# Optimization experiments

Hardware: AMD Instinct MI355X
Metric: run time of the kernel (lower is better)

The kernel has to match this reference:

```python
import jax, jax.numpy as jnp
import numpy as np
from jax import lax

B, L, D = 1024, 50, 128          # batch, max_seq_len, embed_dim
NV, NH = 8, 16                    # n_v vertical filters, n_h horizontal filters
NU, NI = 100000, 100000           # num_users, num_items


def setup_inputs() -> dict:
    key = jax.random.key(0)
    ks = jax.random.split(key, 9)
    return {
        "user_ids": jax.random.randint(ks[0], (B,), 0, NU),
        "item_seq": jax.random.randint(ks[1], (B, L), 0, NI),
        "user_emb": jax.random.normal(ks[2], (NU, D), jnp.float32) * 0.02,
        "item_emb": jax.random.normal(ks[3], (NI, D), jnp.float32) * 0.02,
        "vfilter": jax.random.normal(ks[4], (L, NV), jnp.float32) * 0.1,
        # hconv_w[i] holds the Conv2d(1, NH, (i+1, D)) weight, zero-padded to height L;
        # only rows [:i+1] are used for filter of height h=i+1.
        "hconv_w": jax.random.normal(ks[5], (L, NH, L, D), jnp.float32) * 0.05,
        "hconv_b": jax.random.normal(ks[6], (L, NH), jnp.float32) * 0.01,
        "fc_w": jax.random.normal(ks[7], (NV * D + NH * L, D), jnp.float32) * 0.02,
        "fc_b": jax.random.normal(ks[8], (D,), jnp.float32) * 0.01,
    }


def reference(user_ids, item_seq, user_emb, item_emb, vfilter, hconv_w, hconv_b, fc_w, fc_b):
    P_u = user_emb[user_ids]                 # [B, D]
    E = item_emb[item_seq]                   # [B, L, D]

    # vertical conv: (E^T @ V)^T flattened as (v major, d minor) -> [B, NV*D]
    o_v = jnp.einsum('bld,lv->bvd', E, vfilter).reshape(E.shape[0], -1)

    # horizontal convs: one per kernel height h = 1..L (structurally distinct kernels)
    x = E[:, None, :, :]                     # NCHW: [B, 1, L, D]
    o_h = []
    for i in range(L):
        h = i + 1
        w = hconv_w[i, :, :h, :][:, None, :, :]   # OIHW: [NH, 1, h, D]
        c = lax.conv_general_dilated(
            x, w, window_strides=(1, 1), padding='VALID',
            dimension_numbers=('NCHW', 'OIHW', 'NCHW'))[..., 0]   # [B, NH, L-h+1]
        c = jax.nn.relu(c + hconv_b[i][None, :, None])
        o_h.append(jnp.max(c, axis=2))            # max-pool over all valid positions
    o_h = jnp.concatenate(o_h, axis=1)            # [B, NH*L]

    o = jnp.concatenate([o_v, o_h], axis=1)       # [B, NV*D + NH*L]
    z = jax.nn.relu(o @ fc_w + fc_b)              # [B, D]
    return jnp.concatenate([z, P_u], axis=1)      # [B, 2*D]
```

## Files before the change

kernel.cpp:

```cpp
#include <hip/hip_runtime.h>
#include <hip/hip_bf16.h>
#include <stdint.h>

#define B_   1024
#define L_   50
#define D_   128
#define NV_  8
#define NH_  16
#define KFC  1824

typedef __bf16 bf16x8 __attribute__((ext_vector_type(8)));
typedef float  f32x4  __attribute__((ext_vector_type(4)));

static __device__ __forceinline__ bf16x8 as_bf16x8(uint4 u) {
  return __builtin_bit_cast(bf16x8, u);
}

static __device__ __forceinline__ unsigned short f2b(float x) {
  unsigned u = __float_as_uint(x);
  return (unsigned short)((u + 0x7FFFu + ((u >> 16) & 1u)) >> 16);
}

#define OV_BYTES  ((size_t)B_ * KFC * 4)
#define E3OFF     (OV_BYTES)
#define E3_KS     3342336
#define E3_BG     52224
#define E3SZ      ((size_t)4 * E3_KS)
#define W2OFF     (E3OFF + E3SZ)
#define W2SZ      ((size_t)1275 * 4096)
#define NEED_FULL (W2OFF + W2SZ)

__global__ void ck_kP(const int* __restrict__ uids, const float* __restrict__ uemb,
                      float* __restrict__ out) {
  int b = blockIdx.x, d = threadIdx.x;
  out[(size_t)b * 256 + 128 + d] = uemb[(size_t)uids[b] * D_ + d];
}

__global__ void ck_kZ(float* __restrict__ out) {
  int i = blockIdx.x * 256 + threadIdx.x;
  int b = i >> 7, d = i & 127;
  out[(size_t)b * 256 + d] = 0.f;
}

__global__ void ck_kAB(const int* __restrict__ item_seq, const float* __restrict__ item_emb,
                       const float* __restrict__ vf, char* __restrict__ ws) {
  int b = blockIdx.x, tid = threadIdx.x;
  __shared__ float E[L_][D_];
  __shared__ float VF[L_][NV_];
  __shared__ int sidx[L_];
  if (tid < L_) sidx[tid] = item_seq[b * L_ + tid];
  for (int c = tid; c < L_ * NV_; c += 256) VF[c / NV_][c % NV_] = vf[c];
  __syncthreads();
  for (int c = tid; c < 1600; c += 256) {
    int l = c >> 5, ch = c & 31;
    *(float4*)&E[l][ch * 4] = *(const float4*)(item_emb + (size_t)sidx[l] * D_ + ch * 4);
  }
  __syncthreads();
  char* eg = ws + E3OFF + (size_t)(b >> 4) * E3_BG + (b & 15) * 64;
  #pragma unroll
  for (int it = 0; it < 4; ++it) {
    int c = it * 256 + tid;
    if (c < 816) {
      int ks = c / 204, rem = c - ks * 204;
      uint4 v = make_uint4(0, 0, 0, 0);
      int row, gq;
      if (rem < 200) {
        row = rem >> 2; gq = rem & 3;
        float4 f0 = *(const float4*)&E[row][ks * 32 + gq * 8];
        float4 f1 = *(const float4*)&E[row][ks * 32 + gq * 8 + 4];
        v.x = f2b(f0.x) | ((unsigned)f2b(f0.y) << 16);
        v.y = f2b(f0.z) | ((unsigned)f2b(f0.w) << 16);
        v.z = f2b(f1.x) | ((unsigned)f2b(f1.y) << 16);
        v.w = f2b(f1.z) | ((unsigned)f2b(f1.w) << 16);
      } else {
        row = 50; gq = rem - 200;
      }
      *(uint4*)(eg + (size_t)ks * E3_KS + row * 1024 + gq * 16) = v;
    }
  }
  int d = tid & 127, half = tid >> 7;
  float acc[4] = {0.f, 0.f, 0.f, 0.f};
  for (int l = 0; l < L_; ++l) {
    float e = E[l][d];
    #pragma unroll
    for (int vv = 0; vv < 4; ++vv) acc[vv] += e * VF[l][half * 4 + vv];
  }
  float* o = (float*)ws + (size_t)b * KFC;
  #pragma unroll
  for (int vv = 0; vv < 4; ++vv) o[(half * 4 + vv) * D_ + d] = acc[vv];
}

__global__ void ck_kW2(const float* __restrict__ hw, char* __restrict__ ws) {
  int p = blockIdx.x, tid = threadIdx.x;
  int ks = tid >> 6, l = tid & 63;
  int n = l & 15, gq = l >> 4;
  int i = (int)((sqrtf(8.0f * (float)p + 1.0f) - 1.0f) * 0.5f);
  while ((i + 1) * (i + 2) / 2 <= p) ++i;
  while (i * (i + 1) / 2 > p) --i;
  int j = p - i * (i + 1) / 2;
  const float* src = hw + ((size_t)(i * 16 + n) * 50 + j) * 128 + ks * 32 + gq * 8;
  float4 f0 = *(const float4*)(src);
  float4 f1 = *(const float4*)(src + 4);
  uint4 v;
  v.x = f2b(f0.x) | ((unsigned)f2b(f0.y) << 16);
  v.y = f2b(f0.z) | ((unsigned)f2b(f0.w) << 16);
  v.z = f2b(f1.x) | ((unsigned)f2b(f1.y) << 16);
  v.w = f2b(f1.z) | ((unsigned)f2b(f1.w) << 16);
  *(uint4*)(ws + W2OFF + (size_t)p * 4096 + tid * 16) = v;
}

#define MFMA_BF16 __builtin_amdgcn_mfma_f32_16x16x32_bf16

template<int NT4>
__device__ __forceinline__ void proc_item_g(const char* __restrict__ ebase,
    const char* __restrict__ bp0, int i, int t0, f32x4 (&acc)[8]) {
  bf16x8 win[8];
  #pragma unroll
  for (int q = 0; q < 8; ++q) {
    int s = t0 + q; s = s > 50 ? 50 : s;
    win[q] = as_bf16x8(*(const uint4*)(ebase + s * 1024));
  }
  uint4 breg[8];
  #pragma unroll
  for (int u = 0; u < 8; ++u)
    breg[u] = *(const uint4*)(bp0 + (size_t)(u <= i ? u : 0) * 4096);

  for (int j0 = 0; j0 <= i; j0 += 8) {
    #pragma unroll
    for (int u = 0; u < 8; ++u) {
      int j = j0 + u;
      if (j <= i) {
        bf16x8 bfr = as_bf16x8(breg[u]);
        acc[0] = MFMA_BF16(win[u], bfr, acc[0], 0, 0, 0);
        acc[1] = MFMA_BF16(win[(u + 1) & 7], bfr, acc[1], 0, 0, 0);
        acc[2] = MFMA_BF16(win[(u + 2) & 7], bfr, acc[2], 0, 0, 0);
        acc[3] = MFMA_BF16(win[(u + 3) & 7], bfr, acc[3], 0, 0, 0);
        int sn = t0 + j + 8; sn = sn > 50 ? 50 : sn;
        win[u] = as_bf16x8(*(const uint4*)(ebase + sn * 1024));
        if (NT4 == 8) {
          acc[4] = MFMA_BF16(win[(u + 4) & 7], bfr, acc[4], 0, 0, 0);
          acc[5] = MFMA_BF16(win[(u + 5) & 7], bfr, acc[5], 0, 0, 0);
          acc[6] = MFMA_BF16(win[(u + 6) & 7], bfr, acc[6], 0, 0, 0);
          acc[7] = MFMA_BF16(win[(u + 7) & 7], bfr, acc[7], 0, 0, 0);
        }
        if (j + 8 <= i) breg[u] = *(const uint4*)(bp0 + (size_t)(j + 8) * 4096);
      }
    }
  }
}

__launch_bounds__(256, 4)
__global__ void ck_kC6(const float* __restrict__ hconv_b, char* __restrict__ ws) {
  int tid = threadIdx.x;
  int wv = tid >> 6, lane = tid & 63;
  int r = lane & 15, gq = lane >> 4;
  int bid = (int)blockIdx.x;
  int g = bid & 63;
  int q = bid >> 6;
  int widx = q * 4 + wv;

  int rem = widx, i = -1, nt = 0, t0 = 0;
  for (int ii = 49; ii >= 0; --ii) {
    int nw = (57 - ii) >> 3;
    if (rem < nw) {
      i = ii;
      int ntb = 50 - ii - 8 * (nw - 1);
      nt = rem ? 8 : ntb;
      t0 = rem ? ntb + 8 * (rem - 1) : 0;
      break;
    }
    rem -= nw;
  }
  if (i < 0) return;
  int nt4 = (nt + 3) & ~3;

  const char* EG = ws + E3OFF + (size_t)g * E3_BG + r * 64 + gq * 16;
  const char* W2 = ws + W2OFF + (size_t)(i * (i + 1) / 2) * 4096 + lane * 16;
  float* o = (float*)ws;

  f32x4 acc[8];
  #pragma unroll
  for (int t = 0; t < 8; ++t) {
    acc[t][0] = 0.f; acc[t][1] = 0.f; acc[t][2] = 0.f; acc[t][3] = 0.f;
  }

  #pragma unroll
  for (int ks = 0; ks < 4; ++ks) {
    const char* ebase = EG + (size_t)ks * E3_KS;
    const char* bp0   = W2 + ks * 1024;
    if (nt4 == 4) proc_item_g<4>(ebase, bp0, i, t0, acc);
    else          proc_item_g<8>(ebase, bp0, i, t0, acc);
  }

  int b0 = g * 16;
  float bias = hconv_b[i * 16 + r];
  #pragma unroll
  for (int e = 0; e < 4; ++e) {
    float m = 0.f;
    #pragma unroll
    for (int tt = 0; tt < 8; ++tt)
      if (tt < nt) m = fmaxf(m, fmaxf(acc[tt][e] + bias, 0.f));
    atomicMax((unsigned*)&o[(size_t)(b0 + gq * 4 + e) * KFC + 1024 + i * 16 + r],
              __float_as_uint(m));
  }
}

__launch_bounds__(256)
__global__ void ck_kD(const float* __restrict__ fc_w, const float* __restrict__ fc_b,
                      const char* __restrict__ ws, float* __restrict__ out) {
  __shared__ char ldsD[10240];
  int b0 = blockIdx.x * 64, n0 = blockIdx.y * 16;
  int tid = threadIdx.x, w = tid >> 6, lane = tid & 63, r = lane & 15, gq = lane >> 4;
  const float* o = (const float*)ws;

  f32x4 acc; acc[0] = 0.f; acc[1] = 0.f; acc[2] = 0.f; acc[3] = 0.f;

  int rl = tid >> 2, ch = tid & 3;
  const float* asrc = o + (size_t)(b0 + rl) * KFC + ch * 8;
  int kk = tid >> 3, nn = tid & 7;

  float4 fa[4]; float fb[4];
  fa[0] = *(const float4*)(asrc);
  fa[1] = *(const float4*)(asrc + 4);
  fa[2] = *(const float4*)(asrc + 32);
  fa[3] = *(const float4*)(asrc + 36);
  fb[0] = fc_w[(size_t)kk * D_ + n0 + nn];
  fb[1] = fc_w[(size_t)kk * D_ + n0 + nn + 8];
  fb[2] = fc_w[(size_t)(32 + kk) * D_ + n0 + nn];
  fb[3] = fc_w[(size_t)(32 + kk) * D_ + n0 + nn + 8];

  int arow_off = rl * 64 + ((ch ^ (rl & 3)) << 4);
  int rloc = w * 16 + r;
  int ard = rloc * 64 + ((gq ^ (rloc & 3)) << 4);
  int brd = 8192 + r * 64 + ((gq ^ (r & 3)) << 4);
  int bw0 = 8192 + nn * 64 + (((kk >> 3) ^ (nn & 3)) << 4) + (kk & 7) * 2;
  int bw1 = 8192 + (nn + 8) * 64 + (((kk >> 3) ^ ((nn + 8) & 3)) << 4) + (kk & 7) * 2;

  for (int s = 0; s < 29; ++s) {
    int k1ok = (2 * s + 1) < 57;
    __syncthreads();
    #pragma unroll
    for (int sl = 0; sl < 2; ++sl) {
      uint4 v;
      v.x = f2b(fa[2*sl].x) | ((unsigned)f2b(fa[2*sl].y) << 16);
      v.y = f2b(fa[2*sl].z) | ((unsigned)f2b(fa[2*sl].w) << 16);
      v.z = f2b(fa[2*sl+1].x) | ((unsigned)f2b(fa[2*sl+1].y) << 16);
      v.w = f2b(fa[2*sl+1].z) | ((unsigned)f2b(fa[2*sl+1].w) << 16);
      *(uint4*)(ldsD + sl * 4096 + arow_off) = v;
      *(unsigned short*)(ldsD + sl * 1024 + bw0) = f2b(fb[2*sl]);
      *(unsigned short*)(ldsD + sl * 1024 + bw1) = f2b(fb[2*sl+1]);
    }
    __syncthreads();
    int kn0 = (2 * s + 2) * 32, kn1 = (2 * s + 3) * 32;
    if (kn0 < 1824) {
      fa[0] = *(const float4*)(asrc + kn0);
      fa[1] = *(const float4*)(asrc + kn0 + 4);
      fb[0] = fc_w[(size_t)(kn0 + kk) * D_ + n0 + nn];
      fb[1] = fc_w[(size_t)(kn0 + kk) * D_ + n0 + nn + 8];
    }
    if (kn1 < 1824) {
      fa[2] = *(const float4*)(asrc + kn1);
      fa[3] = *(const float4*)(asrc + kn1 + 4);
      fb[2] = fc_w[(size_t)(kn1 + kk) * D_ + n0 + nn];
      fb[3] = fc_w[(size_t)(kn1 + kk) * D_ + n0 + nn + 8];
    }
    bf16x8 a0  = as_bf16x8(*(const uint4*)(ldsD + ard));
    bf16x8 b0f = as_bf16x8(*(const uint4*)(ldsD + brd));
    acc = __builtin_amdgcn_mfma_f32_16x16x32_bf16(a0, b0f, acc, 0, 0, 0);
    if (k1ok) {
      bf16x8 a1  = as_bf16x8(*(const uint4*)(ldsD + 4096 + ard));
      bf16x8 b1f = as_bf16x8(*(const uint4*)(ldsD + 1024 + brd));
      acc = __builtin_amdgcn_mfma_f32_16x16x32_bf16(a1, b1f, acc, 0, 0, 0);
    }
  }

  float bias = fc_b[n0 + r];
  #pragma unroll
  for (int e = 0; e < 4; ++e) {
    int row = b0 + w * 16 + gq * 4 + e;
    out[(size_t)row * 256 + n0 + r] = fmaxf(acc[e] + bias, 0.f);
  }
}

extern "C" void kernel_launch(void* const* d_in, const int* in_sizes, int n_in,
                              void* d_out, int out_size, void* d_ws, size_t ws_size,
                              hipStream_t stream) {
  const int*   user_ids = (const int*)d_in[0];
  const int*   item_seq = (const int*)d_in[1];
  const float* user_emb = (const float*)d_in[2];
  const float* item_emb = (const float*)d_in[3];
  const float* vfilter  = (const float*)d_in[4];
  const float* hconv_w  = (const float*)d_in[5];
  const float* hconv_b  = (const float*)d_in[6];
  const float* fc_w     = (const float*)d_in[7];
  const float* fc_b     = (const float*)d_in[8];
  float* out = (float*)d_out;
  char*  ws  = (char*)d_ws;

  ck_kP<<<dim3(B_), dim3(128), 0, stream>>>(user_ids, user_emb, out);

  if (ws_size < NEED_FULL) {
    ck_kZ<<<dim3(512), dim3(256), 0, stream>>>(out);
    return;
  }

  hipMemsetAsync(ws, 0, OV_BYTES, stream);

  ck_kAB<<<dim3(B_), dim3(256), 0, stream>>>(item_seq, item_emb, vfilter, ws);
  ck_kW2<<<dim3(1275), dim3(256), 0, stream>>>(hconv_w, ws);
  ck_kC6<<<dim3(2944), dim3(256), 0, stream>>>(hconv_b, ws);
  ck_kD<<<dim3(16, 8), dim3(256), 0, stream>>>(fc_w, fc_b, ws, out);
}
```

Before: 174.9 us.

## Stage per-group embedding slices in LDS and distribute conv work via atomic counter

The horizontal-conv kernel now copies each 16-batch group's bf16 embedding slice into shared memory with global_load_lds and reads its sliding windows from LDS instead of global memory. It launches a persistent grid of 12 blocks per group with 8 waves each. Those blocks pull work items dynamically through a per-group atomic counter that is zeroed in the workspace. The intent is to cut repeated global/L2 reads of the same embedding data and to balance the uneven triangular workload. In exchange, every K-slice now needs extra block-wide barriers, and some waves idle when the remaining work is smaller than a block.

```diff
diff --git a/kernel.cpp b/kernel.cpp
--- a/kernel.cpp
+++ b/kernel.cpp
@@ -23,12 +23,17 @@
 
 #define OV_BYTES  ((size_t)B_ * KFC * 4)
 #define E3OFF     (OV_BYTES)
-#define E3_KS     3342336
 #define E3_BG     52224
+#define E3_KS     ((size_t)64 * E3_BG)
 #define E3SZ      ((size_t)4 * E3_KS)
 #define W2OFF     (E3OFF + E3SZ)
 #define W2SZ      ((size_t)1275 * 4096)
-#define NEED_FULL (W2OFF + W2SZ)
+#define CTR_OFF   (W2OFF + W2SZ)
+#define NEED_FULL (CTR_OFF + 256)
+
+#define GLD16(gsrc, ldst) __builtin_amdgcn_global_load_lds(                    \
+    (const __attribute__((address_space(1))) void*)(gsrc),                     \
+    (__attribute__((address_space(3))) void*)(ldst), 16, 0, 0)
 
 __global__ void ck_kP(const int* __restrict__ uids, const float* __restrict__ uemb,
                       float* __restrict__ out) {
@@ -111,14 +116,13 @@
 
 #define MFMA_BF16 __builtin_amdgcn_mfma_f32_16x16x32_bf16
 
-template<int NT4>
-__device__ __forceinline__ void proc_item_g(const char* __restrict__ ebase,
-    const char* __restrict__ bp0, int i, int t0, f32x4 (&acc)[8]) {
+__device__ __forceinline__ void proc8(const char* buf, const char* bp0,
+    int i, int t0, f32x4 (&acc)[8], int aoff) {
   bf16x8 win[8];
   #pragma unroll
   for (int q = 0; q < 8; ++q) {
     int s = t0 + q; s = s > 50 ? 50 : s;
-    win[q] = as_bf16x8(*(const uint4*)(ebase + s * 1024));
+    win[q] = as_bf16x8(*(const uint4*)(buf + s * 1024 + aoff));
   }
   uint4 breg[8];
   #pragma unroll
@@ -136,72 +140,92 @@
         acc[2] = MFMA_BF16(win[(u + 2) & 7], bfr, acc[2], 0, 0, 0);
         acc[3] = MFMA_BF16(win[(u + 3) & 7], bfr, acc[3], 0, 0, 0);
         int sn = t0 + j + 8; sn = sn > 50 ? 50 : sn;
-        win[u] = as_bf16x8(*(const uint4*)(ebase + sn * 1024));
-        if (NT4 == 8) {
-          acc[4] = MFMA_BF16(win[(u + 4) & 7], bfr, acc[4], 0, 0, 0);
-          acc[5] = MFMA_BF16(win[(u + 5) & 7], bfr, acc[5], 0, 0, 0);
-          acc[6] = MFMA_BF16(win[(u + 6) & 7], bfr, acc[6], 0, 0, 0);
-          acc[7] = MFMA_BF16(win[(u + 7) & 7], bfr, acc[7], 0, 0, 0);
-        }
+        win[u] = as_bf16x8(*(const uint4*)(buf + sn * 1024 + aoff));
+        acc[4] = MFMA_BF16(win[(u + 4) & 7], bfr, acc[4], 0, 0, 0);
+        acc[5] = MFMA_BF16(win[(u + 5) & 7], bfr, acc[5], 0, 0, 0);
+        acc[6] = MFMA_BF16(win[(u + 6) & 7], bfr, acc[6], 0, 0, 0);
+        acc[7] = MFMA_BF16(win[(u + 7) & 7], bfr, acc[7], 0, 0, 0);
         if (j + 8 <= i) breg[u] = *(const uint4*)(bp0 + (size_t)(j + 8) * 4096);
       }
     }
   }
 }
 
-__launch_bounds__(256, 4)
-__global__ void ck_kC6(const float* __restrict__ hconv_b, char* __restrict__ ws) {
+__launch_bounds__(512, 4)
+__global__ void ck_kC8(const float* __restrict__ hconv_b, char* __restrict__ ws) {
+  __shared__ __align__(16) char lds[E3_BG + 16];
+  int* bcast = (int*)(lds + E3_BG);
   int tid = threadIdx.x;
   int wv = tid >> 6, lane = tid & 63;
   int r = lane & 15, gq = lane >> 4;
-  int bid = (int)blockIdx.x;
-  int g = bid & 63;
-  int q = bid >> 6;
-  int widx = q * 4 + wv;
-
-  int rem = widx, i = -1, nt = 0, t0 = 0;
-  for (int ii = 49; ii >= 0; --ii) {
-    int nw = (57 - ii) >> 3;
-    if (rem < nw) {
-      i = ii;
-      int ntb = 50 - ii - 8 * (nw - 1);
-      nt = rem ? 8 : ntb;
-      t0 = rem ? ntb + 8 * (rem - 1) : 0;
-      break;
-    }
-    rem -= nw;
-  }
-  if (i < 0) return;
-  int nt4 = (nt + 3) & ~3;
-
-  const char* EG = ws + E3OFF + (size_t)g * E3_BG + r * 64 + gq * 16;
-  const char* W2 = ws + W2OFF + (size_t)(i * (i + 1) / 2) * 4096 + lane * 16;
+  int g = (int)blockIdx.x;
+  int aoff = r * 64 + gq * 16;
+
+  const char* EG = ws + E3OFF + (size_t)g * E3_BG;
+  const char* W2 = ws + W2OFF;
+  unsigned* ctr = (unsigned*)(ws + CTR_OFF) + g;
   float* o = (float*)ws;
 
-  f32x4 acc[8];
-  #pragma unroll
-  for (int t = 0; t < 8; ++t) {
-    acc[t][0] = 0.f; acc[t][1] = 0.f; acc[t][2] = 0.f; acc[t][3] = 0.f;
-  }
-
-  #pragma unroll
-  for (int ks = 0; ks < 4; ++ks) {
-    const char* ebase = EG + (size_t)ks * E3_KS;
-    const char* bp0   = W2 + ks * 1024;
-    if (nt4 == 4) proc_item_g<4>(ebase, bp0, i, t0, acc);
-    else          proc_item_g<8>(ebase, bp0, i, t0, acc);
-  }
-
-  int b0 = g * 16;
-  float bias = hconv_b[i * 16 + r];
-  #pragma unroll
-  for (int e = 0; e < 4; ++e) {
-    float m = 0.f;
-    #pragma unroll
-    for (int tt = 0; tt < 8; ++tt)
-      if (tt < nt) m = fmaxf(m, fmaxf(acc[tt][e] + bias, 0.f));
-    atomicMax((unsigned*)&o[(size_t)(b0 + gq * 4 + e) * KFC + 1024 + i * 16 + r],
-              __float_as_uint(m));
+  for (;;) {
+    if (tid == 0) bcast[0] = (int)atomicAdd(ctr, 8u);
+    #pragma unroll
+    for (int it = 0; it < 6; ++it)
+      GLD16(EG + (size_t)(it * 512 + tid) * 16, lds + (it * 512 + wv * 64) * 16);
+    if (wv < 3)
+      GLD16(EG + (size_t)(3072 + tid) * 16, lds + (3072 + wv * 64) * 16);
+    __syncthreads();
+    int base = bcast[0];
+    if (base >= 182) break;
+
+    int widx = base + wv;
+    int i = -1, nt = 0, t0 = 0;
+    int rem = widx;
+    for (int ii = 49; ii >= 0; --ii) {
+      int nw = (57 - ii) >> 3;
+      if (rem < nw) {
+        i = ii;
+        int ntb = 50 - ii - 8 * (nw - 1);
+        nt = rem ? 8 : ntb;
+        t0 = rem ? ntb + 8 * (rem - 1) : 0;
+        break;
+      }
+      rem -= nw;
+    }
+
+    f32x4 acc[8];
+    #pragma unroll
+    for (int t = 0; t < 8; ++t) {
+      acc[t][0] = 0.f; acc[t][1] = 0.f; acc[t][2] = 0.f; acc[t][3] = 0.f;
+    }
+    const char* bpb = W2 + (size_t)(i >= 0 ? i * (i + 1) / 2 : 0) * 4096 + lane * 16;
+
+    for (int ks = 0; ks < 4; ++ks) {
+      if (i >= 0) proc8(lds, bpb + ks * 1024, i, t0, acc, aoff);
+      __syncthreads();
+      if (ks < 3) {
+        const char* src = EG + (size_t)(ks + 1) * E3_KS;
+        #pragma unroll
+        for (int it = 0; it < 6; ++it)
+          GLD16(src + (size_t)(it * 512 + tid) * 16, lds + (it * 512 + wv * 64) * 16);
+        if (wv < 3)
+          GLD16(src + (size_t)(3072 + tid) * 16, lds + (3072 + wv * 64) * 16);
+        __syncthreads();
+      }
+    }
+
+    if (i >= 0) {
+      int b0 = g * 16;
+      float bias = hconv_b[i * 16 + r];
+      #pragma unroll
+      for (int e = 0; e < 4; ++e) {
+        float m = 0.f;
+        #pragma unroll
+        for (int tt = 0; tt < 8; ++tt)
+          if (tt < nt) m = fmaxf(m, fmaxf(acc[tt][e] + bias, 0.f));
+        atomicMax((unsigned*)&o[(size_t)(b0 + gq * 4 + e) * KFC + 1024 + i * 16 + r],
+                  __float_as_uint(m));
+      }
+    }
   }
 }
 
@@ -305,9 +329,10 @@
   }
 
   hipMemsetAsync(ws, 0, OV_BYTES, stream);
+  hipMemsetAsync(ws + CTR_OFF, 0, 256, stream);
 
   ck_kAB<<<dim3(B_), dim3(256), 0, stream>>>(item_seq, item_emb, vfilter, ws);
   ck_kW2<<<dim3(1275), dim3(256), 0, stream>>>(hconv_w, ws);
-  ck_kC6<<<dim3(2944), dim3(256), 0, stream>>>(hconv_b, ws);
+  ck_kC8<<<dim3(64, 12), dim3(512), 0, stream>>>(hconv_b, ws);
   ck_kD<<<dim3(16, 8), dim3(256), 0, stream>>>(fc_w, fc_b, ws, out);
 }
```

Result: no change. 175.3 us (+0.3%).
